# Kernel tuning notes

Hardware: AMD Instinct MI355X
Metric: run time of the kernel (lower is better)

## Reference

```python
import jax, jax.numpy as jnp
import numpy as np

HEADS = 8
DIM_HEAD = 128
BUCKET_SIZE = 128


def setup_inputs() -> dict:
    key = jax.random.key(0)
    ks = jax.random.split(key, 5)
    b, t, d = 4, 4096, 1024
    dh_all = HEADS * DIM_HEAD  # 1024
    x = jax.random.normal(ks[0], (b, t, d), dtype=jnp.float32)
    # 0.02 init scale keeps qk logits in a sane range (mimics trained-weight scale)
    Wq = jax.random.normal(ks[1], (d, dh_all), dtype=jnp.float32) * 0.02
    Wkv = jax.random.normal(ks[2], (d, 2 * dh_all), dtype=jnp.float32) * 0.02
    Wo = jax.random.normal(ks[3], (dh_all, d), dtype=jnp.float32) * 0.02
    bo = jnp.zeros((d,), dtype=jnp.float32)
    return {"x": x, "Wq": Wq, "Wkv": Wkv, "Wo": Wo, "bo": bo}


def reference(x, Wq, Wkv, Wo, bo):
    b, t, d = x.shape
    h, dh, bs = HEADS, DIM_HEAD, BUCKET_SIZE
    buckets = t // bs
    scale = dh ** -0.5

    # projections (Linear without bias for q/kv)
    q = x @ Wq                      # [b, t, h*dh]
    k, v = jnp.split(x @ Wkv, 2, axis=-1)

    def merge_heads(u):             # [b, t, h*dh] -> [b*h, t, dh]
        return u.reshape(b, t, h, dh).transpose(0, 2, 1, 3).reshape(b * h, t, dh)

    q, k, v = merge_heads(q), merge_heads(k), merge_heads(v)

    # bucket: [b*h, buckets, bs, dh]
    bq = q.reshape(b * h, buckets, bs, dh)
    bk = k.reshape(b * h, buckets, bs, dh)
    bv = v.reshape(b * h, buckets, bs, dh)

    # AttentionSortNet (non_permutative=True): bucket-mean similarity -> softmax
    sq = bq.mean(axis=2)            # [b*h, buckets, dh]
    sk = bk.mean(axis=2)
    R = jnp.einsum('bie,bje->bij', sq, sk) * scale
    R = jax.nn.softmax(R, axis=-1)  # [b*h, buckets, buckets]

    # soft-reorder kv buckets and concat with local buckets (n_sortcut == 0)
    bk_r = jnp.einsum('buv,bvtd->butd', R, bk)
    bv_r = jnp.einsum('buv,bvtd->butd', R, bv)
    bk_cat = jnp.concatenate([bk_r, bk], axis=2)   # [b*h, buckets, 2*bs, dh]
    bv_cat = jnp.concatenate([bv_r, bv], axis=2)

    # per-bucket attention
    dots = jnp.einsum('buie,buje->buij', bq, bk_cat) * scale
    attn = jax.nn.softmax(dots, axis=-1)
    out = jnp.einsum('buij,buje->buie', attn, bv_cat)  # [b*h, buckets, bs, dh]

    # unbucket + split heads back: [b, t, h*dh]
    out = out.reshape(b, h, t, dh).transpose(0, 2, 1, 3).reshape(b, t, h * dh)
    return out @ Wo + bo
```

## Files before the change

kernel.cpp:

```cpp
#include <hip/hip_runtime.h>
#include <hip/hip_bf16.h>
#include <stdint.h>

typedef short short8 __attribute__((ext_vector_type(8)));
typedef float f32x4 __attribute__((ext_vector_type(4)));

__device__ __forceinline__ unsigned short f2bf(float f) {
    unsigned u = __float_as_uint(f);
    u += 0x7fff + ((u >> 16) & 1);
    return (unsigned short)(u >> 16);
}
__device__ __forceinline__ float bf2f(unsigned short h) {
    return __uint_as_float(((unsigned)h) << 16);
}

__device__ __forceinline__ void gload_lds16(const void* g, void* l) {
    __builtin_amdgcn_global_load_lds(
        (const __attribute__((address_space(1))) void*)g,
        (__attribute__((address_space(3))) void*)l, 16, 0, 0);
}

__global__ void cast_x_kernel(const float* __restrict__ x, unsigned short* __restrict__ xb, int n) {
    int i = (blockIdx.x * blockDim.x + threadIdx.x) * 4;
    int stride = gridDim.x * blockDim.x * 4;
    for (; i < n; i += stride) {
        float4 f = *(const float4*)(x + i);
        ushort4 o;
        o.x = f2bf(f.x); o.y = f2bf(f.y); o.z = f2bf(f.z); o.w = f2bf(f.w);
        *(ushort4*)(xb + i) = o;
    }
}

__global__ void transpose_cast_kernel(const float* __restrict__ W, unsigned short* __restrict__ Wt,
                                      int K, int N) {
    __shared__ unsigned short tile[32][33];
    int k0 = blockIdx.x * 32, n0 = blockIdx.y * 32;
    int tx = threadIdx.x & 31, ty = threadIdx.x >> 5;
#pragma unroll
    for (int i = 0; i < 32; i += 8)
        tile[ty + i][tx] = f2bf(W[(size_t)(k0 + ty + i) * N + n0 + tx]);
    __syncthreads();
#pragma unroll
    for (int i = 0; i < 32; i += 8)
        Wt[(size_t)(n0 + ty + i) * K + k0 + tx] = tile[tx][ty + i];
}

template <int MODE>
__global__ __launch_bounds__(512, 2)
void gemmP(const unsigned short* __restrict__ A, const unsigned short* __restrict__ B,
           unsigned short* __restrict__ obf, float* __restrict__ of,
           const float* __restrict__ bias) {
    __shared__ unsigned short Ssh[65536];
    const int tid = threadIdx.x;
    const int w = tid >> 6, lane = tid & 63;
    const int lr = lane & 15, lg = lane >> 4, r7 = lane & 7;
    const int wr = w >> 2, wc = w & 3;
    const int orig = blockIdx.x;
    const int lgc = (orig & 7) * 32 + (orig >> 3);
    const int m0 = (lgc >> 2) * 256, n0 = (lgc & 3) * 256;
    const int srow8 = lane >> 3;
    const int sgrp = (lane & 7) ^ srow8;
    const unsigned short* gA = A + (size_t)(m0 + w * 16 + srow8) * 1024 + sgrp * 8;
    const unsigned short* gB = B + (size_t)(n0 + w * 16 + srow8) * 1024 + sgrp * 8;

    f32x4 acc[8][4] = {};

#define SH(BUF, HALF, KT) {                                                              \
        const unsigned short* gp_ = ((HALF) < 2 ? gA : gB) +                             \
                                    (size_t)(((HALF) & 1) * 128) * 1024 + (KT);          \
        unsigned short* lp_ = Ssh + ((HALF) < 2 ? 0 : 32768) + (BUF) * 16384 +           \
                              ((HALF) & 1) * 8192 + w * 1024;                            \
        gload_lds16(gp_, lp_);                                                           \
        gload_lds16(gp_ + 8192, lp_ + 512);                                              \
    }

    SH(0, 0, 0) SH(0, 1, 0) SH(0, 2, 0) SH(0, 3, 0)
    SH(1, 0, 64) SH(1, 1, 64) SH(1, 2, 64) SH(1, 3, 64)
    asm volatile("s_waitcnt vmcnt(8)" ::: "memory");
    __builtin_amdgcn_sched_barrier(0);
    __builtin_amdgcn_s_barrier();

#pragma unroll 2
    for (int t = 0; t < 16; ++t) {
        const int cur = t & 1;
        const unsigned short* Ab = Ssh + cur * 16384;
        const unsigned short* Bb = Ssh + 32768 + cur * 16384;
        short8 af[8][2], bf[4][2];

#pragma unroll
        for (int mi = 0; mi < 4; ++mi)
#pragma unroll
            for (int kk = 0; kk < 2; ++kk)
                af[mi][kk] = *(const short8*)(Ab + (wr * 128 + mi * 16 + lr) * 64 +
                                              (((kk << 2) | lg) ^ r7) * 8);
#pragma unroll
        for (int ni = 0; ni < 2; ++ni)
#pragma unroll
            for (int kk = 0; kk < 2; ++kk)
                bf[ni][kk] = *(const short8*)(Bb + (wc * 64 + ni * 16 + lr) * 64 +
                                              (((kk << 2) | lg) ^ r7) * 8);
        __builtin_amdgcn_sched_barrier(0);
#pragma unroll
        for (int mi = 4; mi < 8; ++mi)
#pragma unroll
            for (int kk = 0; kk < 2; ++kk)
                af[mi][kk] = *(const short8*)(Ab + (wr * 128 + mi * 16 + lr) * 64 +
                                              (((kk << 2) | lg) ^ r7) * 8);
#pragma unroll
        for (int ni = 2; ni < 4; ++ni)
#pragma unroll
            for (int kk = 0; kk < 2; ++kk)
                bf[ni][kk] = *(const short8*)(Bb + (wc * 64 + ni * 16 + lr) * 64 +
                                              (((kk << 2) | lg) ^ r7) * 8);
        __builtin_amdgcn_sched_barrier(0);

        asm volatile("s_waitcnt lgkmcnt(12)" ::: "memory");
        __builtin_amdgcn_sched_barrier(0);
        __builtin_amdgcn_s_setprio(1);
#pragma unroll
        for (int mi = 0; mi < 4; ++mi)
#pragma unroll
            for (int ni = 0; ni < 2; ++ni)
#pragma unroll
                for (int kk = 0; kk < 2; ++kk)
                    acc[mi][ni] = __builtin_amdgcn_mfma_f32_16x16x32_bf16(af[mi][kk], bf[ni][kk],
                                                                          acc[mi][ni], 0, 0, 0);
        __builtin_amdgcn_s_setprio(0);

        asm volatile("s_waitcnt lgkmcnt(0)" ::: "memory");
        __builtin_amdgcn_sched_barrier(0);
        __builtin_amdgcn_s_barrier();
        if (t + 2 < 16) {
            const int kt2 = (t + 2) * 64;
            SH(cur, 0, kt2) SH(cur, 1, kt2) SH(cur, 2, kt2) SH(cur, 3, kt2)
        }

        __builtin_amdgcn_s_setprio(1);
#pragma unroll
        for (int mi = 4; mi < 8; ++mi)
#pragma unroll
            for (int ni = 0; ni < 2; ++ni)
#pragma unroll
                for (int kk = 0; kk < 2; ++kk)
                    acc[mi][ni] = __builtin_amdgcn_mfma_f32_16x16x32_bf16(af[mi][kk], bf[ni][kk],
                                                                          acc[mi][ni], 0, 0, 0);
#pragma unroll
        for (int mi = 0; mi < 8; ++mi)
#pragma unroll
            for (int ni = 2; ni < 4; ++ni)
#pragma unroll
                for (int kk = 0; kk < 2; ++kk)
                    acc[mi][ni] = __builtin_amdgcn_mfma_f32_16x16x32_bf16(af[mi][kk], bf[ni][kk],
                                                                          acc[mi][ni], 0, 0, 0);
        __builtin_amdgcn_s_setprio(0);

        if (t < 14) {
            asm volatile("s_waitcnt vmcnt(8)" ::: "memory");
            __builtin_amdgcn_sched_barrier(0);
        } else if (t == 14) {
            asm volatile("s_waitcnt vmcnt(0)" ::: "memory");
            __builtin_amdgcn_sched_barrier(0);
        }
        __builtin_amdgcn_s_barrier();
    }
#undef SH

#pragma unroll
    for (int mi = 0; mi < 8; ++mi)
#pragma unroll
        for (int ni = 0; ni < 4; ++ni) {
            if (MODE == 2) {
                int gm0 = m0 + wr * 128 + mi * 16 + lg * 4;
                int gn = n0 + wc * 64 + ni * 16 + lr;
                int b = gm0 >> 12, tt0 = gm0 & 4095, h = gn >> 7, dl = gn & 127;
                int u = tt0 >> 7, tl0 = tt0 & 127;
                size_t base = (size_t)(b * 8 + h) * 524288 + (size_t)u * 16384 + dl * 128 + tl0;
#pragma unroll
                for (int r = 0; r < 4; r += 2) {
                    unsigned pk = (unsigned)f2bf(acc[mi][ni][r]) |
                                  ((unsigned)f2bf(acc[mi][ni][r + 1]) << 16);
                    *(unsigned*)(obf + base + r) = pk;
                }
            } else {
#pragma unroll
                for (int r = 0; r < 4; ++r) {
                    int gm = m0 + wr * 128 + mi * 16 + lg * 4 + r;
                    int gn = n0 + wc * 64 + ni * 16 + lr;
                    float val = acc[mi][ni][r];
                    if (MODE == 3) {
                        of[(size_t)gm * 1024 + gn] = val + bias[gn];
                    } else {
                        int b = gm >> 12, tt = gm & 4095, h = gn >> 7, dl = gn & 127;
                        if (MODE == 0) {
                            obf[(size_t)(b * 8 + h) * 524288 + (size_t)tt * 128 + dl] =
                                f2bf(val * 0.08838834764831845f);
                        } else {
                            obf[(size_t)(b * 8 + h) * 524288 + (size_t)tt * 128 + dl] = f2bf(val);
                        }
                    }
                }
            }
        }

    if (MODE == 0 || MODE == 1) {
#pragma unroll
        for (int ni = 0; ni < 4; ++ni) {
            float ssum = 0.f;
#pragma unroll
            for (int mi = 0; mi < 8; ++mi)
#pragma unroll
                for (int r = 0; r < 4; ++r) ssum += acc[mi][ni][r];
            ssum += __shfl_xor(ssum, 16);
            ssum += __shfl_xor(ssum, 32);
            if (lane < 16) {
                int gn = n0 + wc * 64 + ni * 16 + lr;
                int h = gn >> 7, dl = gn & 127;
                int bh = (m0 >> 12) * 8 + h;
                int u = ((m0 & 4095) >> 7) + wr;
                const float sc = (MODE == 0) ? (0.08838834764831845f / 128.f) : (1.f / 128.f);
                of[(size_t)(bh * 32 + u) * 128 + dl] = ssum * sc;
            }
        }
    }
}

__global__ void sortnet_kernel(const float* __restrict__ sq, const float* __restrict__ sk,
                               float* __restrict__ R) {
    __shared__ float qs[32 * 129];
    __shared__ float ks[32 * 129];
    int bh = blockIdx.x, tid = threadIdx.x;
    for (int i = tid; i < 4096; i += 1024) {
        int row = i >> 7, col = i & 127;
        qs[row * 129 + col] = sq[(size_t)bh * 4096 + i];
        ks[row * 129 + col] = sk[(size_t)bh * 4096 + i];
    }
    __syncthreads();
    int u = tid >> 5, v = tid & 31;
    float dot = 0.f;
    for (int d = 0; d < 128; ++d) dot += qs[u * 129 + d] * ks[v * 129 + d];
    float mx = dot;
    for (int m = 16; m >= 1; m >>= 1) mx = fmaxf(mx, __shfl_xor(mx, m, 32));
    float e = __expf(dot - mx);
    float s = e;
    for (int m = 16; m >= 1; m >>= 1) s += __shfl_xor(s, m, 32);
    R[(size_t)bh * 1024 + u * 32 + v] = e / s;
}

__global__ __launch_bounds__(256)
void mix_kernel(const unsigned short* __restrict__ k, const unsigned short* __restrict__ vT,
                const float* __restrict__ R, unsigned short* __restrict__ bkr,
                unsigned short* __restrict__ bvrT) {
    __shared__ float Rs[1024];
    int bh = blockIdx.x >> 6, chunk = blockIdx.x & 63;
    int tid = threadIdx.x;
    for (int i = tid; i < 1024; i += 256) Rs[i] = R[(size_t)bh * 1024 + i];
    __syncthreads();
    int e = chunk * 256 + tid;
    size_t base = (size_t)bh * 524288 + e;
    float kv_[32], vv[32];
#pragma unroll
    for (int vb = 0; vb < 32; ++vb) {
        kv_[vb] = bf2f(k[base + (size_t)vb * 16384]);
        vv[vb] = bf2f(vT[base + (size_t)vb * 16384]);
    }
    for (int u = 0; u < 32; ++u) {
        float aK = 0.f, aV = 0.f;
#pragma unroll
        for (int vb = 0; vb < 32; ++vb) {
            float r = Rs[u * 32 + vb];
            aK += r * kv_[vb];
            aV += r * vv[vb];
        }
        bkr[(size_t)bh * 524288 + (size_t)u * 16384 + e] = f2bf(aK);
        bvrT[(size_t)bh * 524288 + (size_t)u * 16384 + e] = f2bf(aV);
    }
}

__global__ __launch_bounds__(512)
void attn_kernel(const unsigned short* __restrict__ q, const unsigned short* __restrict__ k,
                 const unsigned short* __restrict__ vT, const unsigned short* __restrict__ bkr,
                 const unsigned short* __restrict__ bvrT, unsigned short* __restrict__ ao) {
    __shared__ unsigned short KB[2][8192];
    __shared__ unsigned short VB[2][8192];
    __shared__ unsigned short Ps[8][1024];
    const int orig = blockIdx.x;
    const int bid = (orig & 7) * 128 + (orig >> 3);
    const int bh = bid >> 5, u = bid & 31;
    const int tid = threadIdx.x, w = tid >> 6, lane = tid & 63;
    const int lr = lane & 15, lg = lane >> 4;
    const size_t bb = (size_t)bh * 524288 + (size_t)u * 16384;

#define STAGE_K(SRC, BUF)                                                        \
    _Pragma("unroll")                                                            \
    for (int i = 0; i < 2; ++i) {                                                \
        const int row_ = i * 32 + (tid >> 4);                                    \
        gload_lds16((SRC) + row_ * 128 + (((tid & 15) ^ (row_ & 7)) * 8),        \
                    (char*)KB[BUF] + i * 8192 + tid * 16);                       \
    }
#define STAGE_V(SRC, BUF)                                                        \
    _Pragma("unroll")                                                            \
    for (int i = 0; i < 2; ++i) {                                                \
        const int row_ = i * 64 + (tid >> 3);                                    \
        gload_lds16((SRC) + row_ * 128 + (((tid & 7) ^ (row_ & 7)) * 8),         \
                    (char*)VB[BUF] + i * 8192 + tid * 16);                       \
    }

    const unsigned short* qg = q + bb + (size_t)(w * 16) * 128;
    short8 aq[4];
#pragma unroll
    for (int kk = 0; kk < 4; ++kk)
        aq[kk] = *(const short8*)(qg + lr * 128 + kk * 32 + lg * 8);

    STAGE_K(bkr + bb, 0) STAGE_V(bvrT + bb, 0)
    STAGE_K(bkr + bb + 8192, 1) STAGE_V(bvrT + bb + 64, 1)

    short8 ones8;
#pragma unroll
    for (int i = 0; i < 8; ++i) ones8[i] = (short)0x3F80;

    f32x4 oacc[8] = {};
    f32x4 lacc = {};

    asm volatile("s_waitcnt vmcnt(4)" ::: "memory");
    __builtin_amdgcn_sched_barrier(0);
    __builtin_amdgcn_s_barrier();

    unsigned short* Pw = Ps[w];

#pragma unroll
    for (int c = 0; c < 4; ++c) {
        const int cb = c & 1;
        f32x4 s[4] = {};
        __builtin_amdgcn_s_setprio(1);
#pragma unroll
        for (int kk = 0; kk < 4; ++kk)
#pragma unroll
            for (int ni = 0; ni < 4; ++ni) {
                short8 kb8 = *(const short8*)(&KB[cb][(ni * 16 + lr) * 128 +
                                              (((kk * 4 + lg) ^ (lr & 7)) * 8)]);
                s[ni] = __builtin_amdgcn_mfma_f32_16x16x32_bf16(aq[kk], kb8, s[ni], 0, 0, 0);
            }
        __builtin_amdgcn_s_setprio(0);

#pragma unroll
        for (int r = 0; r < 4; ++r) {
            int prow = lg * 4 + r;
#pragma unroll
            for (int ni = 0; ni < 4; ++ni)
                Pw[prow * 64 + ((ni * 16 + lr) ^ ((prow & 7) << 3))] = f2bf(__expf(s[ni][r]));
        }

        __builtin_amdgcn_s_setprio(1);
#pragma unroll
        for (int ks2 = 0; ks2 < 2; ++ks2) {
            short8 ap = *(const short8*)(&Pw[lr * 64 + ((ks2 * 32 + lg * 8) ^ ((lr & 7) << 3))]);
            lacc = __builtin_amdgcn_mfma_f32_16x16x32_bf16(ap, ones8, lacc, 0, 0, 0);
#pragma unroll
            for (int ni = 0; ni < 8; ++ni) {
                short8 bv8 = *(const short8*)(&VB[cb][(ni * 16 + lr) * 64 +
                                              (((ks2 * 4 + lg) ^ (lr & 7)) * 8)]);
                oacc[ni] = __builtin_amdgcn_mfma_f32_16x16x32_bf16(ap, bv8, oacc[ni], 0, 0, 0);
            }
        }
        __builtin_amdgcn_s_setprio(0);

        __builtin_amdgcn_s_barrier();
        if (c == 0) { STAGE_K(k + bb, 0) STAGE_V(vT + bb, 0) }
        else if (c == 1) { STAGE_K(k + bb + 8192, 1) STAGE_V(vT + bb + 64, 1) }
        if (c < 2) {
            asm volatile("s_waitcnt vmcnt(4)" ::: "memory");
            __builtin_amdgcn_sched_barrier(0);
            __builtin_amdgcn_s_barrier();
        } else if (c == 2) {
            asm volatile("s_waitcnt vmcnt(0)" ::: "memory");
            __builtin_amdgcn_sched_barrier(0);
            __builtin_amdgcn_s_barrier();
        }
    }

    const int b = bh >> 3, h = bh & 7;
#pragma unroll
    for (int r = 0; r < 4; ++r) {
        int row = w * 16 + lg * 4 + r;
        size_t rowbase = ((size_t)b * 4096 + u * 128 + row) * 1024 + h * 128;
        float inv = 1.f / lacc[r];
#pragma unroll
        for (int ni = 0; ni < 8; ++ni)
            ao[rowbase + ni * 16 + lr] = f2bf(oacc[ni][r] * inv);
    }
#undef STAGE_K
#undef STAGE_V
}

extern "C" void kernel_launch(void* const* d_in, const int* in_sizes, int n_in,
                              void* d_out, int out_size, void* d_ws, size_t ws_size,
                              hipStream_t stream) {
    (void)in_sizes; (void)n_in; (void)out_size; (void)ws_size;
    const float* x   = (const float*)d_in[0];
    const float* Wq  = (const float*)d_in[1];
    const float* Wkv = (const float*)d_in[2];
    const float* Wo  = (const float*)d_in[3];
    const float* bo  = (const float*)d_in[4];
    float* out = (float*)d_out;

    char* ws = (char*)d_ws;
    const size_t SZ_BIG = 33554432;
    unsigned short* xb    = (unsigned short*)(ws);
    unsigned short* qb    = (unsigned short*)(ws + SZ_BIG);
    unsigned short* kb    = (unsigned short*)(ws + 2 * SZ_BIG);
    unsigned short* vtb   = (unsigned short*)(ws + 3 * SZ_BIG);
    unsigned short* bkr   = (unsigned short*)(ws + 4 * SZ_BIG);
    unsigned short* bvrT  = (unsigned short*)(ws + 5 * SZ_BIG);
    size_t off = 6 * SZ_BIG;
    unsigned short* wqkvt = (unsigned short*)(ws + off); off += 6291456;
    unsigned short* wot   = (unsigned short*)(ws + off); off += 2097152;
    float* sq   = (float*)(ws + off); off += 524288;
    float* sk   = (float*)(ws + off); off += 524288;
    float* Rbuf = (float*)(ws + off); off += 131072;

    cast_x_kernel<<<4096, 256, 0, stream>>>(x, xb, 16777216);
    transpose_cast_kernel<<<dim3(32, 32), 256, 0, stream>>>(Wq, wqkvt, 1024, 1024);
    transpose_cast_kernel<<<dim3(32, 64), 256, 0, stream>>>(Wkv, wqkvt + 1048576, 1024, 2048);
    transpose_cast_kernel<<<dim3(32, 32), 256, 0, stream>>>(Wo, wot, 1024, 1024);

    gemmP<0><<<256, 512, 0, stream>>>(xb, wqkvt,           qb,  sq, nullptr);
    gemmP<1><<<256, 512, 0, stream>>>(xb, wqkvt + 1048576, kb,  sk, nullptr);
    gemmP<2><<<256, 512, 0, stream>>>(xb, wqkvt + 2097152, vtb, nullptr, nullptr);

    sortnet_kernel<<<32, 1024, 0, stream>>>(sq, sk, Rbuf);
    mix_kernel<<<2048, 256, 0, stream>>>(kb, vtb, Rbuf, bkr, bvrT);

    attn_kernel<<<1024, 512, 0, stream>>>(qb, kb, vtb, bkr, bvrT, xb);

    gemmP<3><<<256, 512, 0, stream>>>(xb, wot, nullptr, out, bo);
}
```

Before: 272.1 us.

## Restructure mix kernel: split K/V per block, pack pairs, read R directly

The mix kernel now assigns K and V to separate blocks and has each thread handle two adjacent bf16 elements through 32-bit loads and stores. It accumulates into packed float2 values across four independent accumulators. R is read straight from global memory as float4 (uniform, cacheable) instead of being staged through shared memory with a barrier. The aim is fewer, wider memory transactions, more instruction-level parallelism and better occupancy, at the cost of more registers per thread and redundant R reads across blocks.

```diff
diff --git a/kernel.cpp b/kernel.cpp
--- a/kernel.cpp
+++ b/kernel.cpp
@@ -4,6 +4,7 @@
 
 typedef short short8 __attribute__((ext_vector_type(8)));
 typedef float f32x4 __attribute__((ext_vector_type(4)));
+typedef float f32x2 __attribute__((ext_vector_type(2)));
 
 __device__ __forceinline__ unsigned short f2bf(float f) {
     unsigned u = __float_as_uint(f);
@@ -246,33 +247,53 @@
     R[(size_t)bh * 1024 + u * 32 + v] = e / s;
 }
 
-__global__ __launch_bounds__(256)
+__global__ __launch_bounds__(256, 4)
 void mix_kernel(const unsigned short* __restrict__ k, const unsigned short* __restrict__ vT,
                 const float* __restrict__ R, unsigned short* __restrict__ bkr,
                 unsigned short* __restrict__ bvrT) {
-    __shared__ float Rs[1024];
-    int bh = blockIdx.x >> 6, chunk = blockIdx.x & 63;
-    int tid = threadIdx.x;
-    for (int i = tid; i < 1024; i += 256) Rs[i] = R[(size_t)bh * 1024 + i];
-    __syncthreads();
-    int e = chunk * 256 + tid;
-    size_t base = (size_t)bh * 524288 + e;
-    float kv_[32], vv[32];
-#pragma unroll
-    for (int vb = 0; vb < 32; ++vb) {
-        kv_[vb] = bf2f(k[base + (size_t)vb * 16384]);
-        vv[vb] = bf2f(vT[base + (size_t)vb * 16384]);
-    }
+    const int bid = blockIdx.x;
+    const int arr = bid & 1;
+    const int rest = bid >> 1;
+    const int bh = rest >> 5, chunk = rest & 31;
+    const int tid = threadIdx.x;
+    const unsigned short* __restrict__ src = arr ? vT : k;
+    unsigned short* __restrict__ dst = arr ? bvrT : bkr;
+    const float* __restrict__ Rb = R + (size_t)bh * 1024;
+
+    const int e = chunk * 512 + tid * 2;
+    const size_t base = (size_t)bh * 524288 + e;
+
+    unsigned raw[32];
+#pragma unroll
+    for (int vb = 0; vb < 32; ++vb)
+        raw[vb] = *(const unsigned*)(src + base + (size_t)vb * 16384);
+    f32x2 val[32];
+#pragma unroll
+    for (int vb = 0; vb < 32; ++vb)
+        val[vb] = f32x2{bf2f((unsigned short)raw[vb]), bf2f((unsigned short)(raw[vb] >> 16))};
+
+#pragma unroll 2
     for (int u = 0; u < 32; ++u) {
-        float aK = 0.f, aV = 0.f;
-#pragma unroll
-        for (int vb = 0; vb < 32; ++vb) {
-            float r = Rs[u * 32 + vb];
-            aK += r * kv_[vb];
-            aV += r * vv[vb];
-        }
-        bkr[(size_t)bh * 524288 + (size_t)u * 16384 + e] = f2bf(aK);
-        bvrT[(size_t)bh * 524288 + (size_t)u * 16384 + e] = f2bf(aV);
+        f32x2 a0 = {0.f, 0.f}, a1 = {0.f, 0.f}, a2 = {0.f, 0.f}, a3 = {0.f, 0.f};
+#pragma unroll
+        for (int g = 0; g < 2; ++g) {
+            float4 r0 = *(const float4*)(Rb + u * 32 + g * 16);
+            float4 r1 = *(const float4*)(Rb + u * 32 + g * 16 + 4);
+            float4 r2 = *(const float4*)(Rb + u * 32 + g * 16 + 8);
+            float4 r3 = *(const float4*)(Rb + u * 32 + g * 16 + 12);
+            const int b0 = g * 16;
+            a0 += r0.x * val[b0 + 0];  a0 += r0.y * val[b0 + 1];
+            a0 += r0.z * val[b0 + 2];  a0 += r0.w * val[b0 + 3];
+            a1 += r1.x * val[b0 + 4];  a1 += r1.y * val[b0 + 5];
+            a1 += r1.z * val[b0 + 6];  a1 += r1.w * val[b0 + 7];
+            a2 += r2.x * val[b0 + 8];  a2 += r2.y * val[b0 + 9];
+            a2 += r2.z * val[b0 + 10]; a2 += r2.w * val[b0 + 11];
+            a3 += r3.x * val[b0 + 12]; a3 += r3.y * val[b0 + 13];
+            a3 += r3.z * val[b0 + 14]; a3 += r3.w * val[b0 + 15];
+        }
+        f32x2 a = (a0 + a1) + (a2 + a3);
+        unsigned o = (unsigned)f2bf(a.x) | ((unsigned)f2bf(a.y) << 16);
+        *(unsigned*)(dst + (size_t)bh * 524288 + (size_t)u * 16384 + e) = o;
     }
 }
 
```

New measurement: 262.0 us. 3.7% less time.
